# Performance work log

Hardware: AMD Instinct MI355X
Metric: run time of the kernel (lower is better)

The kernel has to match this reference:

```python
import jax, jax.numpy as jnp
import numpy as np
import math

B, T, D, V, M = 32, 2048, 512, 4096, 64
COVERAGE_FLOOR = 0.05
BIG = 1e30


def masked_median(values, mask):
    # values, mask: [B, T]; torch.median = lower median = sorted[(n-1)//2]
    valid = mask > 0.5
    n = valid.sum(axis=1)  # [B]
    s = jnp.sort(jnp.where(valid, values, BIG), axis=1)
    idx = jnp.maximum((n - 1) // 2, 0)
    med = jnp.take_along_axis(s, idx[:, None], axis=1)  # [B,1]
    return jnp.where(n[:, None] > 0, med, 0.0)


def masked_mean(values, mask):
    # values: [B,T,D], mask: [B,T]
    denom = jnp.maximum(mask.sum(axis=1, keepdims=True), 1.0)  # [B,1]
    return (values * mask[:, :, None]).sum(axis=1) / denom


def masked_std(values, mask, mean):
    denom = jnp.maximum(mask.sum(axis=1, keepdims=True), 1.0)
    diff2 = (values - mean[:, None, :]) ** 2 * mask[:, :, None]
    return jnp.sqrt(diff2.sum(axis=1) / jnp.maximum(denom, 1e-6) + 1e-6)


def conv1d(x, w, b):
    # x: [B,T,D], w: [K=3, I=D, O=D], padding=1 -> same length
    y = jax.lax.conv_general_dilated(x, w, window_strides=(1,), padding=[(1, 1)],
                                     dimension_numbers=('NHC', 'HIO', 'NHC'))
    return y + b


def layer_norm(x, w, b, eps=1e-5):
    mu = x.mean(axis=-1, keepdims=True)
    var = ((x - mu) ** 2).mean(axis=-1, keepdims=True)
    return (x - mu) * jax.lax.rsqrt(var + eps) * w + b


def setup_inputs() -> dict:
    key = jax.random.key(0)
    ks = jax.random.split(key, 20)
    units = jax.random.randint(ks[0], (B, T), 0, V)
    dur = jax.random.uniform(ks[1], (B, T), jnp.float32, 0.01, 2.0)
    valid = (jax.random.uniform(ks[2], (B, T)) > 0.1).astype(jnp.float32)
    speech = valid * (jax.random.uniform(ks[3], (B, T)) > 0.2).astype(jnp.float32)
    s = 0.02
    params = dict(
        emb=jax.random.normal(ks[4], (V, D)) * s,
        W_in=jax.random.normal(ks[5], (D + 2, D)) * s, b_in=jnp.zeros((D,)),
        W_c1=jax.random.normal(ks[6], (3, D, D)) * s, b_c1=jnp.zeros((D,)),
        W_c2=jax.random.normal(ks[7], (3, D, D)) * s, b_c2=jnp.zeros((D,)),
        ln_w=jnp.ones((D,)), ln_b=jnp.zeros((D,)),
        codebook_key=jax.random.normal(ks[8], (M, D)) * s,
        W_p1=jax.random.normal(ks[9], (2 * D, D)) * s, b_p1=jnp.zeros((D,)),
        W_p2=jax.random.normal(ks[10], (D, D)) * s, b_p2=jnp.zeros((D,)),
    )
    return dict(prompt_content_units=units, prompt_duration_obs=dur,
                prompt_valid_mask=valid, prompt_speech_mask=speech, **params)


def reference(prompt_content_units, prompt_duration_obs, prompt_valid_mask, prompt_speech_mask,
              emb, W_in, b_in, W_c1, b_c1, W_c2, b_c2, ln_w, ln_b,
              codebook_key, W_p1, b_p1, W_p2, b_p2):
    valid = jnp.clip(prompt_valid_mask, 0.0, 1.0)          # [B,T]
    speech = jnp.clip(prompt_speech_mask, 0.0, 1.0) * valid
    logdur = jnp.log(jnp.maximum(prompt_duration_obs, 1e-4)) * valid
    global_rate = masked_median(logdur, speech)             # [B,1]
    ref_residual = (logdur - global_rate) * valid            # [B,T]

    # encode prompt summary
    sil_flag = jnp.maximum(valid - speech, 0.0)
    h = jnp.concatenate([emb[prompt_content_units],
                         ref_residual[:, :, None], sil_flag[:, :, None]], axis=-1)
    h = h @ W_in + b_in                                      # [B,T,D]
    h = jax.nn.gelu(conv1d(h, W_c1, b_c1), approximate=False)
    h = jax.nn.gelu(conv1d(h, W_c2, b_c2), approximate=False)
    h = layer_norm(h, ln_w, ln_b) * valid[:, :, None]

    summary_mask = speech  # summary_pool_speech_only=True
    mean = masked_mean(h, summary_mask)                      # [B,D]
    std = masked_std(h, summary_mask, mean)                  # [B,D]
    z = jnp.concatenate([mean, std], axis=-1) @ W_p1 + b_p1
    summary_state = jnp.tanh(jax.nn.gelu(z, approximate=False) @ W_p2 + b_p2)
    support_raw = valid.sum(axis=1, keepdims=True)           # [B,1]
    support = jnp.maximum(support_raw, 1.0)
    summary_state = jnp.where(support_raw > 0.0, summary_state, 0.0)

    score = jnp.einsum('btd,md->btm', h, codebook_key) / math.sqrt(float(D))
    score = jnp.where(valid[:, :, None] <= 0.0, -10000.0, score)
    attn = jax.nn.softmax(score, axis=-1) * valid[:, :, None]  # [B,T,M]
    role_mass = attn.sum(axis=1)                               # [B,M]
    role_denom = jnp.maximum(role_mass, 1e-6)
    role_value = jnp.einsum('btm,bt->bm', attn, ref_residual) / role_denom
    diff2 = (ref_residual[:, :, None] - role_value[:, None, :]) ** 2  # [B,T,M]
    role_var = (attn * diff2).sum(axis=1) / role_denom
    role_var = jnp.maximum(jnp.where(role_mass > 0.0, role_var, 1e-4), 1e-4)
    role_coverage = jnp.maximum(role_mass / support, COVERAGE_FLOOR)
    prompt_role_fit = jnp.einsum('btm,bm->bt', attn, role_value) * valid

    return (global_rate, summary_state, role_value, role_var, role_coverage, prompt_role_fit)
```

## Files before the change

### kernel.cpp

```cpp
#include <hip/hip_runtime.h>
#include <hip/hip_bf16.h>
#include <math.h>


typedef unsigned short u16;
typedef unsigned char u8;
typedef __attribute__((ext_vector_type(8))) short short8;
typedef __attribute__((ext_vector_type(4))) float f32x4;
typedef __attribute__((ext_vector_type(4))) int int4v;
typedef __attribute__((ext_vector_type(8))) int int8v;

constexpr int B_ = 32, T_ = 2048, D_ = 512, V_ = 4096, M_ = 64, TP_ = 2050;

constexpr int OUT_GR = 0;
constexpr int OUT_SUM = 32;
constexpr int OUT_RV = 16416;
constexpr int OUT_VAR = 18464;
constexpr int OUT_COV = 20512;
constexpr int OUT_FIT = 22560;

constexpr size_t OFF_S0 = 0;
constexpr size_t OFF_S1 = OFF_S0 + 2048 * 4;
constexpr size_t OFF_S2 = OFF_S1 + 2048 * 4;
constexpr size_t OFF_SH = OFF_S2 + 2048 * 4;
constexpr size_t OFF_SH2 = OFF_SH + 16384 * 4;
constexpr size_t ZERO_BYTES = OFF_SH2 + 16384 * 4;
constexpr size_t OFF_RESID = ZERO_BYTES;
constexpr size_t OFF_GR = OFF_RESID + 65536 * 4;
constexpr size_t OFF_SUP = OFF_GR + 128;
constexpr size_t OFF_SPC = OFF_SUP + 128;
constexpr size_t OFF_RVW = OFF_SPC + 128;
constexpr size_t OFF_WTIN = OFF_RVW + 8192;
constexpr size_t OFF_WTC1 = OFF_WTIN + 524288;
constexpr size_t OFF_WTC2 = OFF_WTC1 + 786432;
constexpr size_t OFF_CKB = OFF_WTC2 + 786432;
constexpr size_t OFF_EMBB = OFF_CKB + 65536;
constexpr size_t OFF_TBL = OFF_EMBB + 4194304;
constexpr size_t OFF_H0 = OFF_TBL + 8388608;
constexpr size_t OFF_H1 = OFF_H0 + 33587200;
constexpr size_t OFF_H2 = OFF_H1 + 33587200;
constexpr size_t OFF_ATTN = OFF_H2 + 67108864;

__device__ __forceinline__ float clamp01(float x) { return fminf(fmaxf(x, 0.f), 1.f); }
__device__ __forceinline__ float b2f(u16 u) { return __uint_as_float(((unsigned)u) << 16); }
__device__ __forceinline__ u16 f2b(float f) {
  unsigned u = __float_as_uint(f);
  unsigned r = (u + 0x7FFFu + ((u >> 16) & 1u)) >> 16;
  return (u16)r;
}
__device__ __forceinline__ u8 f2fp8(float f) {
  return (u8)(__builtin_amdgcn_cvt_pk_fp8_f32(f, f, 0, false) & 0xFF);
}
__device__ __forceinline__ float gelu_f(float x) {
  return 0.5f * x * (1.0f + erff(x * 0.7071067811865475f));
}
__device__ __forceinline__ void gload16(const void* g, void* l) {
  __builtin_amdgcn_global_load_lds((const __attribute__((address_space(1))) void*)g,
                                   (__attribute__((address_space(3))) void*)l, 16, 0, 0);
}

__global__ __launch_bounds__(256) void median_kernel(
    const float* __restrict__ dur, const float* __restrict__ vmask,
    const float* __restrict__ smask, float* __restrict__ out0,
    float* __restrict__ gr, float* __restrict__ sup, float* __restrict__ spc,
    float* __restrict__ resid) {
  int b = blockIdx.x, tid = threadIdx.x;
  int wv = tid >> 6, lane = tid & 63;
  __shared__ float wredf[8];
  __shared__ int wredi[4];
  unsigned keys[8];
  float ldv[8], vmv[8];
  float vs = 0.f, ss = 0.f;
#pragma unroll
  for (int j = 0; j < 8; ++j) {
    int t = j * 256 + tid;
    float vm = clamp01(vmask[b * T_ + t]);
    float sm = clamp01(smask[b * T_ + t]) * vm;
    vs += vm; ss += sm;
    float ld = logf(fmaxf(dur[b * T_ + t], 1e-4f)) * vm;
    ldv[j] = ld; vmv[j] = vm;
    unsigned bits = __float_as_uint(ld);
    unsigned key = (bits & 0x80000000u) ? ~bits : (bits | 0x80000000u);
    keys[j] = (sm > 0.5f) ? key : 0xFFFFFFFFu;
  }
  for (int o = 32; o > 0; o >>= 1) { vs += __shfl_xor(vs, o); ss += __shfl_xor(ss, o); }
  if (lane == 0) { wredf[wv] = vs; wredf[4 + wv] = ss; }
  __syncthreads();
  float s_sup = wredf[0] + wredf[1] + wredf[2] + wredf[3];
  float s_spc = wredf[4] + wredf[5] + wredf[6] + wredf[7];
  int n = (int)(s_spc + 0.5f);
  int target = (n > 0) ? ((n - 1) / 2 + 1) : 1;
  unsigned lo = 0u, hi = 0xFFFFFFFFu;
  for (int it = 0; it < 32; ++it) {
    unsigned mid = lo + ((hi - lo) >> 1);
    int c = 0;
#pragma unroll
    for (int j = 0; j < 8; ++j) c += (keys[j] <= mid) ? 1 : 0;
    for (int o = 32; o > 0; o >>= 1) c += __shfl_xor(c, o);
    __syncthreads();
    if (lane == 0) wredi[wv] = c;
    __syncthreads();
    int tot = wredi[0] + wredi[1] + wredi[2] + wredi[3];
    if (tot >= target) hi = mid; else lo = mid + 1;
  }
  float med = 0.f;
  if (n > 0) {
    unsigned K = lo;
    unsigned ub = (K & 0x80000000u) ? (K & 0x7FFFFFFFu) : ~K;
    med = __uint_as_float(ub);
  }
  if (tid == 0) { out0[OUT_GR + b] = med; gr[b] = med; sup[b] = s_sup; spc[b] = s_spc; }
#pragma unroll
  for (int j = 0; j < 8; ++j) {
    int t = j * 256 + tid;
    resid[b * T_ + t] = (ldv[j] - med) * vmv[j];
  }
}

__global__ __launch_bounds__(256) void wpack_kernel(
    const float* __restrict__ W_in, const float* __restrict__ W_c1,
    const float* __restrict__ W_c2, u16* __restrict__ wtin,
    u8* __restrict__ wtc1, u8* __restrict__ wtc2) {
  __shared__ float tile[64][65];
  int x = blockIdx.x;
  int m = x >> 6, tl = x & 63;
  int kt = tl >> 3, nt = tl & 7;
  const float* src;
  if (m == 0) src = W_in;
  else if (m <= 3) src = W_c1 + (size_t)(m - 1) * 262144;
  else src = W_c2 + (size_t)(m - 4) * 262144;
  int tid = threadIdx.x;
#pragma unroll
  for (int j = 0; j < 16; ++j) {
    int idx = j * 256 + tid;
    int r = idx >> 6, c = idx & 63;
    tile[r][c] = src[(size_t)(kt * 64 + r) * 512 + nt * 64 + c];
  }
  __syncthreads();
  if (m == 0) {
#pragma unroll
    for (int j = 0; j < 16; ++j) {
      int idx = j * 256 + tid;
      int r = idx >> 6, c = idx & 63;
      wtin[(size_t)(nt * 64 + r) * 512 + kt * 64 + c] = f2b(tile[c][r]);
    }
  } else {
    u8* dst = (m <= 3) ? wtc1 + (size_t)(m - 1) * 262144
                       : wtc2 + (size_t)(m - 4) * 262144;
#pragma unroll
    for (int j = 0; j < 16; ++j) {
      int idx = j * 256 + tid;
      int r = idx >> 6, c = idx & 63;
      dst[(size_t)(nt * 64 + r) * 512 + kt * 64 + c] = f2fp8(tile[c][r] * 64.f);
    }
  }
}

__global__ __launch_bounds__(256) void convert_kernel(
    const float* __restrict__ ck, const float* __restrict__ emb,
    u16* __restrict__ ckb, u16* __restrict__ embb) {
  int idx = blockIdx.x * 256 + threadIdx.x;
  float4 v;
  u16* dst;
  if (idx < 8192) {
    v = reinterpret_cast<const float4*>(ck)[idx];
    dst = ckb + idx * 4;
  } else {
    int i = idx - 8192;
    v = reinterpret_cast<const float4*>(emb)[i];
    dst = embb + (size_t)i * 4;
  }
  uint2 o;
  o.x = (unsigned)f2b(v.x) | ((unsigned)f2b(v.y) << 16);
  o.y = (unsigned)f2b(v.z) | ((unsigned)f2b(v.w) << 16);
  *reinterpret_cast<uint2*>(dst) = o;
}

__global__ __launch_bounds__(256) void gemm_plain_kernel(
    const u16* __restrict__ A, const u16* __restrict__ Bt,
    const float* __restrict__ bias, u16* __restrict__ Cout) {
  __shared__ u16 ldsA[64 * 64];
  __shared__ u16 ldsB[128 * 64];
  const int tid = threadIdx.x;
  const int row0 = blockIdx.x * 64;
  const int col0 = blockIdx.y * 128;

  f32x4 acc[2][4] = {};
  const int wv = tid >> 6, lane = tid & 63;
  const int wr = (wv >> 1) << 5;
  const int wc = (wv & 1) << 6;
  const int lr = lane & 15, cgrp = lane >> 4;

  const u16* Ab = A + (size_t)row0 * 512;
  const u16* Bb = Bt + (size_t)col0 * 512;
  for (int k0 = 0; k0 < 512; k0 += 64) {
    if (k0) __syncthreads();
#pragma unroll
    for (int j = 0; j < 2; ++j) {
      int ci = j * 256 + tid;
      int r = ci >> 3, s = ci & 7;
      int gs = s ^ (r & 7);
      gload16(Ab + (size_t)r * 512 + k0 + gs * 8, &ldsA[ci * 8]);
    }
#pragma unroll
    for (int j = 0; j < 4; ++j) {
      int ci = j * 256 + tid;
      int r = ci >> 3, s = ci & 7;
      int gs = s ^ (r & 7);
      gload16(Bb + (size_t)r * 512 + k0 + gs * 8, &ldsB[ci * 8]);
    }
    __syncthreads();
#pragma unroll
    for (int kk = 0; kk < 2; ++kk) {
      short8 af[2], bfr[4];
#pragma unroll
      for (int m = 0; m < 2; ++m) {
        int r = wr + m * 16 + lr;
        int s = (kk * 4 + cgrp) ^ (r & 7);
        af[m] = *reinterpret_cast<const short8*>(&ldsA[(r << 6) + (s << 3)]);
      }
#pragma unroll
      for (int n = 0; n < 4; ++n) {
        int r = wc + n * 16 + lr;
        int s = (kk * 4 + cgrp) ^ (r & 7);
        bfr[n] = *reinterpret_cast<const short8*>(&ldsB[(r << 6) + (s << 3)]);
      }
#pragma unroll
      for (int m = 0; m < 2; ++m)
#pragma unroll
        for (int n = 0; n < 4; ++n)
          acc[m][n] = __builtin_amdgcn_mfma_f32_16x16x32_bf16(af[m], bfr[n], acc[m][n], 0, 0, 0);
    }
  }
#pragma unroll
  for (int m = 0; m < 2; ++m)
#pragma unroll
    for (int n = 0; n < 4; ++n)
#pragma unroll
      for (int r = 0; r < 4; ++r) {
        int lrow = wr + m * 16 + (lane >> 4) * 4 + r;
        int lcol = wc + n * 16 + (lane & 15);
        Cout[(size_t)(row0 + lrow) * 512 + col0 + lcol] =
            f2b(acc[m][n][r] + bias[col0 + lcol]);
      }
}

template <int PADOUT>
__global__ __launch_bounds__(256, 3) void conv_gemm_kernel(
    const u8* __restrict__ A, const u8* __restrict__ Bt,
    const float* __restrict__ bias, u8* __restrict__ Cout) {
  __shared__ u8 ldsA[130 * 128];
  __shared__ u8 ldsB[3 * 64 * 128];
  const int tid = threadIdx.x;
  const int id = blockIdx.x;
  const int wg = (id & 7) * 512 + (id >> 3);
  const int rb = wg >> 3, cb = wg & 7;
  const int row0 = rb * 128, col0 = cb * 64;
  const int b = row0 >> 11, t0 = row0 & 2047;
  const size_t aBase = ((size_t)b * TP_ + t0) * 512;
  const size_t oBase = PADOUT ? ((size_t)b * TP_ + 1 + t0) : (size_t)row0;

  f32x4 acc[4][2] = {};
  const int wv = tid >> 6, lane = tid & 63;
  const int wr = (wv >> 1) << 6;
  const int wc = (wv & 1) << 5;
  const int lr = lane & 15, cgrp = lane >> 4;

  const u8* Ab = A + aBase;
#pragma unroll 1
  for (int k0 = 0; k0 < 512; k0 += 128) {
    if (k0) __syncthreads();
#pragma unroll
    for (int j = 0; j < 5; ++j) {
      int ci = j * 256 + tid;
      if (ci < 1040) {
        int r = ci >> 3, s = ci & 7;
        int gs = s ^ (r & 7);
        gload16(Ab + (size_t)r * 512 + k0 + gs * 16, &ldsA[ci * 16]);
      }
    }
#pragma unroll
    for (int j = 0; j < 6; ++j) {
      int ci = j * 256 + tid;
      int r = ci >> 3, s = ci & 7;
      int tap = r >> 6, n = r & 63;
      int gs = s ^ (r & 7);
      gload16(Bt + ((size_t)(tap * 512 + col0 + n)) * 512 + k0 + gs * 16, &ldsB[ci * 16]);
    }
    __syncthreads();
#pragma unroll
    for (int tap = 0; tap < 3; ++tap) {
      int8v af[4], bfr[2];
#pragma unroll
      for (int m = 0; m < 4; ++m) {
        int r = wr + m * 16 + lr + tap;
        int s0 = (2 * cgrp) ^ (r & 7);
        int s1 = (2 * cgrp + 1) ^ (r & 7);
        int4v lo = *reinterpret_cast<const int4v*>(&ldsA[(r << 7) + (s0 << 4)]);
        int4v hi = *reinterpret_cast<const int4v*>(&ldsA[(r << 7) + (s1 << 4)]);
        af[m] = __builtin_shufflevector(lo, hi, 0, 1, 2, 3, 4, 5, 6, 7);
      }
#pragma unroll
      for (int n = 0; n < 2; ++n) {
        int rB = tap * 64 + wc + n * 16 + lr;
        int s0 = (2 * cgrp) ^ (rB & 7);
        int s1 = (2 * cgrp + 1) ^ (rB & 7);
        int4v lo = *reinterpret_cast<const int4v*>(&ldsB[(rB << 7) + (s0 << 4)]);
        int4v hi = *reinterpret_cast<const int4v*>(&ldsB[(rB << 7) + (s1 << 4)]);
        bfr[n] = __builtin_shufflevector(lo, hi, 0, 1, 2, 3, 4, 5, 6, 7);
      }
#pragma unroll
      for (int m = 0; m < 4; ++m)
#pragma unroll
        for (int n = 0; n < 2; ++n)
          acc[m][n] = __builtin_amdgcn_mfma_scale_f32_16x16x128_f8f6f4(
              af[m], bfr[n], acc[m][n], 0, 0, 0, 0x7F7F7F7F, 0, 0x7F7F7F7F);
    }
  }
#pragma unroll
  for (int m = 0; m < 4; ++m)
#pragma unroll
    for (int n = 0; n < 2; ++n)
#pragma unroll
      for (int r = 0; r < 4; ++r) {
        int lrow = wr + m * 16 + (lane >> 4) * 4 + r;
        int lcol = wc + n * 16 + (lane & 15);
        float v = acc[m][n][r] * (1.f / 4096.f) + bias[col0 + lcol];
        v = gelu_f(v);
        Cout[(oBase + lrow) * 512 + col0 + lcol] = f2fp8(v * 64.f);
      }
}

__global__ __launch_bounds__(256) void gather_kernel(
    const int* __restrict__ units, const float* __restrict__ resid,
    const float* __restrict__ vmask, const float* __restrict__ smask,
    const u16* __restrict__ tbl, const float* __restrict__ w512,
    const float* __restrict__ w513, u8* __restrict__ h0p, u8* __restrict__ h1p) {
  int row = blockIdx.x * 4 + (threadIdx.x >> 6);
  int b = row / TP_, tp = row - b * TP_;
  int lane = threadIdx.x & 63;
  size_t o = (size_t)row * 512 + lane * 8;
  if (tp == 0 || tp == TP_ - 1) {
    uint2 z = {0, 0};
    *reinterpret_cast<uint2*>(&h0p[o]) = z;
    *reinterpret_cast<uint2*>(&h1p[o]) = z;
    return;
  }
  int t = tp - 1, g = b * T_ + t;
  float vm = clamp01(vmask[g]);
  float sm = clamp01(smask[g]) * vm;
  float sil = fmaxf(vm - sm, 0.f);
  float rs = resid[g];
  int u = units[g];
  uint4 tv = *reinterpret_cast<const uint4*>(tbl + (size_t)u * 512 + lane * 8);
  float tr[8];
  tr[0] = __uint_as_float(tv.x << 16); tr[1] = __uint_as_float(tv.x & 0xFFFF0000u);
  tr[2] = __uint_as_float(tv.y << 16); tr[3] = __uint_as_float(tv.y & 0xFFFF0000u);
  tr[4] = __uint_as_float(tv.z << 16); tr[5] = __uint_as_float(tv.z & 0xFFFF0000u);
  tr[6] = __uint_as_float(tv.w << 16); tr[7] = __uint_as_float(tv.w & 0xFFFF0000u);
  const float* a = w512 + lane * 8;
  const float* c = w513 + lane * 8;
  float f[8];
#pragma unroll
  for (int j = 0; j < 8; ++j) f[j] = (tr[j] + rs * a[j] + sil * c[j]) * 64.f;
  unsigned lo = __builtin_amdgcn_cvt_pk_fp8_f32(f[0], f[1], 0, false);
  lo = __builtin_amdgcn_cvt_pk_fp8_f32(f[2], f[3], lo, true);
  unsigned hi = __builtin_amdgcn_cvt_pk_fp8_f32(f[4], f[5], 0, false);
  hi = __builtin_amdgcn_cvt_pk_fp8_f32(f[6], f[7], hi, true);
  uint2 val = {lo, hi};
  *reinterpret_cast<uint2*>(&h0p[o]) = val;
}

__global__ __launch_bounds__(256) void lnpool_kernel(
    const u8* __restrict__ hin, u16* __restrict__ hout,
    const float* __restrict__ lnw, const float* __restrict__ lnb,
    const float* __restrict__ vmask, const float* __restrict__ smask,
    float* __restrict__ Sh, float* __restrict__ Sh2) {
  int b = blockIdx.y, chunk = blockIdx.x, tid = threadIdx.x;
  int lane = tid & 63, tof = tid >> 6;
  __shared__ float shA[512], shQ[512];
  shA[tid] = 0.f; shA[tid + 256] = 0.f;
  shQ[tid] = 0.f; shQ[tid + 256] = 0.f;
  __syncthreads();
  int d8 = lane * 8;
  float wv_[8], bv_[8];
#pragma unroll
  for (int j = 0; j < 8; ++j) { wv_[j] = lnw[d8 + j]; bv_[j] = lnb[d8 + j]; }
  float a[8] = {}, q[8] = {};
  const float inv64 = 1.f / 64.f;
  for (int i = 0; i < 32; ++i) {
    int t = chunk * 128 + i * 4 + tof;
    int g = b * T_ + t;
    float vm = clamp01(vmask[g]);
    float sp = clamp01(smask[g]) * vm;
    const u8* p = hin + (size_t)g * 512 + d8;
    uint2 raw = *reinterpret_cast<const uint2*>(p);
    float x[8];
    x[0] = __builtin_amdgcn_cvt_f32_fp8(raw.x, 0) * inv64;
    x[1] = __builtin_amdgcn_cvt_f32_fp8(raw.x, 1) * inv64;
    x[2] = __builtin_amdgcn_cvt_f32_fp8(raw.x, 2) * inv64;
    x[3] = __builtin_amdgcn_cvt_f32_fp8(raw.x, 3) * inv64;
    x[4] = __builtin_amdgcn_cvt_f32_fp8(raw.y, 0) * inv64;
    x[5] = __builtin_amdgcn_cvt_f32_fp8(raw.y, 1) * inv64;
    x[6] = __builtin_amdgcn_cvt_f32_fp8(raw.y, 2) * inv64;
    x[7] = __builtin_amdgcn_cvt_f32_fp8(raw.y, 3) * inv64;
    float s = 0.f, sq = 0.f;
#pragma unroll
    for (int j = 0; j < 8; ++j) { s += x[j]; sq = fmaf(x[j], x[j], sq); }
    for (int o = 32; o > 0; o >>= 1) { s += __shfl_xor(s, o); sq += __shfl_xor(sq, o); }
    float mu = s * (1.f / 512.f);
    float var = fmaxf(sq * (1.f / 512.f) - mu * mu, 0.f);
    float rstd = rsqrtf(var + 1e-5f);
    u16 ob[8];
#pragma unroll
    for (int j = 0; j < 8; ++j) {
      float y = ((x[j] - mu) * rstd * wv_[j] + bv_[j]) * vm;
      ob[j] = f2b(y);
      a[j] = fmaf(y, sp, a[j]);
      q[j] = fmaf(y * y, sp, q[j]);
    }
    uint4 val;
    val.x = (unsigned)ob[0] | ((unsigned)ob[1] << 16);
    val.y = (unsigned)ob[2] | ((unsigned)ob[3] << 16);
    val.z = (unsigned)ob[4] | ((unsigned)ob[5] << 16);
    val.w = (unsigned)ob[6] | ((unsigned)ob[7] << 16);
    *reinterpret_cast<uint4*>(&hout[(size_t)g * 512 + d8]) = val;
  }
#pragma unroll
  for (int j = 0; j < 8; ++j) {
    atomicAdd(&shA[d8 + j], a[j]);
    atomicAdd(&shQ[d8 + j], q[j]);
  }
  __syncthreads();
  atomicAdd(&Sh[b * 512 + tid], shA[tid]);
  atomicAdd(&Sh[b * 512 + tid + 256], shA[tid + 256]);
  atomicAdd(&Sh2[b * 512 + tid], shQ[tid]);
  atomicAdd(&Sh2[b * 512 + tid + 256], shQ[tid + 256]);
}

__global__ __launch_bounds__(256) void score_kernel(
    const u16* __restrict__ h, const u16* __restrict__ ckb,
    const float* __restrict__ resid, const float* __restrict__ vmask,
    u16* __restrict__ attn, float* __restrict__ S0, float* __restrict__ S1,
    float* __restrict__ S2) {
  __shared__ char smem[98304];
  __shared__ float s0s[64], s1s[64], s2s[64];
  u16* ckl = (u16*)smem;
  u16* ldsH = (u16*)(smem + 65536);
  float* attn_lds = (float*)smem;

  const int tid = threadIdx.x;
  const int base = blockIdx.x * 256;
  const int bq = base >> 11;

#pragma unroll
  for (int it = 0; it < 16; ++it) {
    int ci = it * 256 + tid;
    int m = ci >> 6, s = ci & 63;
    int sw = (s & 56) | ((s & 7) ^ (m & 7));
    *reinterpret_cast<uint4*>(&ckl[(m << 9) + (sw << 3)]) =
        *reinterpret_cast<const uint4*>(&ckb[(m << 9) + (s << 3)]);
  }
  if (tid < 64) { s0s[tid] = 0.f; s1s[tid] = 0.f; s2s[tid] = 0.f; }

  const int wv = tid >> 6, lane = tid & 63;
  const int lr = lane & 15, cgrp = lane >> 4;
  const int hi = lane >> 4, lf = lane & 15;
  f32x4 acc[4][4] = {};

  const u16* hb = h + (size_t)base * 512;
  for (int k0 = 0; k0 < 512; k0 += 64) {
    __syncthreads();
#pragma unroll
    for (int j = 0; j < 8; ++j) {
      int ci = j * 256 + tid;
      int r = ci >> 3, s = ci & 7;
      int gs = s ^ (r & 7);
      gload16(hb + (size_t)r * 512 + k0 + gs * 8, &ldsH[ci * 8]);
    }
    __syncthreads();
#pragma unroll
    for (int kk = 0; kk < 2; ++kk) {
      short8 af[4], bfr[4];
#pragma unroll
      for (int m = 0; m < 4; ++m) {
        int r = wv * 64 + m * 16 + lr;
        int s = (kk * 4 + cgrp) ^ (r & 7);
        af[m] = *reinterpret_cast<const short8*>(&ldsH[(r << 6) + (s << 3)]);
      }
#pragma unroll
      for (int n = 0; n < 4; ++n) {
        int r = n * 16 + lr;
        int s = (kk * 4 + cgrp) ^ (r & 7);
        bfr[n] = *reinterpret_cast<const short8*>(&ckl[(r << 9) + k0 + (s << 3)]);
      }
#pragma unroll
      for (int m = 0; m < 4; ++m)
#pragma unroll
        for (int n = 0; n < 4; ++n)
          acc[m][n] = __builtin_amdgcn_mfma_f32_16x16x32_bf16(af[m], bfr[n], acc[m][n], 0, 0, 0);
    }
  }
  __syncthreads();

  const float scale = 0.04419417382415922f;
  float s0p[4] = {0.f, 0.f, 0.f, 0.f};
  float s1p[4] = {0.f, 0.f, 0.f, 0.f};
  float s2p[4] = {0.f, 0.f, 0.f, 0.f};
#pragma unroll
  for (int m = 0; m < 4; ++m) {
#pragma unroll
    for (int rr = 0; rr < 4; ++rr) {
      int tl = wv * 64 + m * 16 + hi * 4 + rr;
      int tg = base + tl;
      float v[4];
#pragma unroll
      for (int n = 0; n < 4; ++n) v[n] = acc[m][n][rr] * scale;
      float mx = fmaxf(fmaxf(v[0], v[1]), fmaxf(v[2], v[3]));
      mx = fmaxf(mx, __shfl_xor(mx, 1));
      mx = fmaxf(mx, __shfl_xor(mx, 2));
      mx = fmaxf(mx, __shfl_xor(mx, 4));
      mx = fmaxf(mx, __shfl_xor(mx, 8));
      float e[4], sum = 0.f;
#pragma unroll
      for (int n = 0; n < 4; ++n) { e[n] = expf(v[n] - mx); sum += e[n]; }
      sum += __shfl_xor(sum, 1);
      sum += __shfl_xor(sum, 2);
      sum += __shfl_xor(sum, 4);
      sum += __shfl_xor(sum, 8);
      float vm = clamp01(vmask[tg]);
      float inv = vm / sum;
      float rs = resid[tg];
#pragma unroll
      for (int n = 0; n < 4; ++n) {
        float aa = e[n] * inv;
        attn_lds[tl * 65 + n * 16 + lf] = aa;
        s0p[n] += aa; s1p[n] += aa * rs; s2p[n] += aa * rs * rs;
      }
    }
  }
#pragma unroll
  for (int n = 0; n < 4; ++n) {
    s0p[n] += __shfl_xor(s0p[n], 16); s0p[n] += __shfl_xor(s0p[n], 32);
    s1p[n] += __shfl_xor(s1p[n], 16); s1p[n] += __shfl_xor(s1p[n], 32);
    s2p[n] += __shfl_xor(s2p[n], 16); s2p[n] += __shfl_xor(s2p[n], 32);
  }
  if (hi == 0) {
#pragma unroll
    for (int n = 0; n < 4; ++n) {
      atomicAdd(&s0s[n * 16 + lf], s0p[n]);
      atomicAdd(&s1s[n * 16 + lf], s1p[n]);
      atomicAdd(&s2s[n * 16 + lf], s2p[n]);
    }
  }
  __syncthreads();
#pragma unroll
  for (int it = 0; it < 8; ++it) {
    int ci = it * 256 + tid;
    int tl = ci >> 3, c8 = (ci & 7) * 8;
    u16 ob[8];
#pragma unroll
    for (int j = 0; j < 8; ++j) ob[j] = f2b(attn_lds[tl * 65 + c8 + j]);
    uint4 val;
    val.x = (unsigned)ob[0] | ((unsigned)ob[1] << 16);
    val.y = (unsigned)ob[2] | ((unsigned)ob[3] << 16);
    val.z = (unsigned)ob[4] | ((unsigned)ob[5] << 16);
    val.w = (unsigned)ob[6] | ((unsigned)ob[7] << 16);
    *reinterpret_cast<uint4*>(&attn[(size_t)(base + tl) * 64 + c8]) = val;
  }
  if (tid < 64) {
    atomicAdd(&S0[bq * 64 + tid], s0s[tid]);
    atomicAdd(&S1[bq * 64 + tid], s1s[tid]);
    atomicAdd(&S2[bq * 64 + tid], s2s[tid]);
  }
}

__global__ __launch_bounds__(64) void role_kernel(
    const float* __restrict__ S0, const float* __restrict__ S1,
    const float* __restrict__ S2, const float* __restrict__ sup,
    float* __restrict__ out, float* __restrict__ rv) {
  int b = blockIdx.x, m = threadIdx.x;
  float mass = S0[b * 64 + m], s1 = S1[b * 64 + m], s2 = S2[b * 64 + m];
  float dn = fmaxf(mass, 1e-6f);
  float v = s1 / dn;
  float var = (s2 - 2.f * v * s1 + v * v * mass) / dn;
  var = fmaxf(var, 1e-4f);
  float support = fmaxf(sup[b], 1.f);
  float cov = fmaxf(mass / support, 0.05f);
  out[OUT_RV + b * 64 + m] = v;
  out[OUT_VAR + b * 64 + m] = var;
  out[OUT_COV + b * 64 + m] = cov;
  rv[b * 64 + m] = v;
}

__global__ __launch_bounds__(512) void mlp_kernel(
    const float* __restrict__ Sh, const float* __restrict__ Sh2,
    const float* __restrict__ spc, const float* __restrict__ sup,
    const float* __restrict__ Wp1, const float* __restrict__ bp1,
    const float* __restrict__ Wp2, const float* __restrict__ bp2,
    float* __restrict__ out) {
  int b = blockIdx.x, j = threadIdx.x;
  __shared__ float ms[1024];
  __shared__ float zg[512];
  float denom = fmaxf(spc[b], 1.0f);
  float mean = Sh[b * 512 + j] / denom;
  float ex2 = Sh2[b * 512 + j] / denom;
  float var = fmaxf(ex2 - mean * mean, 0.f);
  ms[j] = mean;
  ms[512 + j] = sqrtf(var + 1e-6f);
  __syncthreads();
  float z0 = 0.f, z1 = 0.f, z2 = 0.f, z3 = 0.f;
  for (int k = 0; k < 1024; k += 4) {
    z0 = fmaf(ms[k], Wp1[(size_t)k * 512 + j], z0);
    z1 = fmaf(ms[k + 1], Wp1[(size_t)(k + 1) * 512 + j], z1);
    z2 = fmaf(ms[k + 2], Wp1[(size_t)(k + 2) * 512 + j], z2);
    z3 = fmaf(ms[k + 3], Wp1[(size_t)(k + 3) * 512 + j], z3);
  }
  float z = bp1[j] + ((z0 + z1) + (z2 + z3));
  zg[j] = gelu_f(z);
  __syncthreads();
  float o0 = 0.f, o1 = 0.f, o2 = 0.f, o3 = 0.f;
  for (int k = 0; k < 512; k += 4) {
    o0 = fmaf(zg[k], Wp2[(size_t)k * 512 + j], o0);
    o1 = fmaf(zg[k + 1], Wp2[(size_t)(k + 1) * 512 + j], o1);
    o2 = fmaf(zg[k + 2], Wp2[(size_t)(k + 2) * 512 + j], o2);
    o3 = fmaf(zg[k + 3], Wp2[(size_t)(k + 3) * 512 + j], o3);
  }
  float o = bp2[j] + ((o0 + o1) + (o2 + o3));
  float sm = tanhf(o);
  out[OUT_SUM + b * 512 + j] = (sup[b] > 0.f) ? sm : 0.f;
}

__global__ __launch_bounds__(256) void fit_kernel(
    const u16* __restrict__ attn, const float* __restrict__ rv,
    const float* __restrict__ vmask, float* __restrict__ out) {
  int tid = threadIdx.x;
  int wv = tid >> 6, lane = tid & 63;
  int t = blockIdx.x * 4 + wv;
  int b = t >> 11;
  float a = b2f(attn[(size_t)t * 64 + lane]) * rv[b * 64 + lane];
  for (int o = 32; o > 0; o >>= 1) a += __shfl_xor(a, o);
  if (lane == 0) out[OUT_FIT + t] = a * clamp01(vmask[t]);
}

extern "C" void kernel_launch(void* const* d_in, const int* in_sizes, int n_in,
                              void* d_out, int out_size, void* d_ws, size_t ws_size,
                              hipStream_t stream) {
  (void)in_sizes; (void)n_in; (void)out_size; (void)ws_size;
  const int* units = (const int*)d_in[0];
  const float* dur = (const float*)d_in[1];
  const float* vmask = (const float*)d_in[2];
  const float* smask = (const float*)d_in[3];
  const float* emb = (const float*)d_in[4];
  const float* W_in = (const float*)d_in[5];
  const float* b_in = (const float*)d_in[6];
  const float* W_c1 = (const float*)d_in[7];
  const float* b_c1 = (const float*)d_in[8];
  const float* W_c2 = (const float*)d_in[9];
  const float* b_c2 = (const float*)d_in[10];
  const float* ln_w = (const float*)d_in[11];
  const float* ln_b = (const float*)d_in[12];
  const float* ck = (const float*)d_in[13];
  const float* W_p1 = (const float*)d_in[14];
  const float* b_p1 = (const float*)d_in[15];
  const float* W_p2 = (const float*)d_in[16];
  const float* b_p2 = (const float*)d_in[17];
  float* out = (float*)d_out;

  char* w = (char*)d_ws;
  float* S0 = (float*)(w + OFF_S0);
  float* S1 = (float*)(w + OFF_S1);
  float* S2 = (float*)(w + OFF_S2);
  float* Sh = (float*)(w + OFF_SH);
  float* Sh2 = (float*)(w + OFF_SH2);
  float* resid = (float*)(w + OFF_RESID);
  float* gr = (float*)(w + OFF_GR);
  float* sup = (float*)(w + OFF_SUP);
  float* spc = (float*)(w + OFF_SPC);
  float* rv = (float*)(w + OFF_RVW);
  u16* wtin = (u16*)(w + OFF_WTIN);
  u8* wtc1 = (u8*)(w + OFF_WTC1);
  u8* wtc2 = (u8*)(w + OFF_WTC2);
  u16* ckb = (u16*)(w + OFF_CKB);
  u16* embb = (u16*)(w + OFF_EMBB);
  u16* tbl = (u16*)(w + OFF_TBL);
  u8* h0p = (u8*)(w + OFF_H0);
  u8* h1p = (u8*)(w + OFF_H1);
  u8* h2f = (u8*)(w + OFF_H2);
  u16* h2b = (u16*)(w + OFF_H0);
  u16* attn = (u16*)(w + OFF_ATTN);

  hipMemsetAsync(d_ws, 0, ZERO_BYTES, stream);
  median_kernel<<<B_, 256, 0, stream>>>(dur, vmask, smask, out, gr, sup, spc, resid);
  wpack_kernel<<<448, 256, 0, stream>>>(W_in, W_c1, W_c2, wtin, wtc1, wtc2);
  convert_kernel<<<2080, 256, 0, stream>>>(ck, emb, ckb, embb);
  gemm_plain_kernel<<<dim3(64, 4), 256, 0, stream>>>(embb, wtin, b_in, tbl);
  gather_kernel<<<B_ * TP_ / 4, 256, 0, stream>>>(units, resid, vmask, smask, tbl,
                                                  W_in + 512 * 512, W_in + 513 * 512, h0p, h1p);
  conv_gemm_kernel<1><<<4096, 256, 0, stream>>>(h0p, wtc1, b_c1, h1p);
  conv_gemm_kernel<0><<<4096, 256, 0, stream>>>(h1p, wtc2, b_c2, h2f);
  lnpool_kernel<<<dim3(16, 32), 256, 0, stream>>>(h2f, h2b, ln_w, ln_b, vmask, smask, Sh, Sh2);
  score_kernel<<<256, 256, 0, stream>>>(h2b, ckb, resid, vmask, attn, S0, S1, S2);
  role_kernel<<<B_, 64, 0, stream>>>(S0, S1, S2, sup, out, rv);
  mlp_kernel<<<B_, 512, 0, stream>>>(Sh, Sh2, spc, sup, W_p1, b_p1, W_p2, b_p2, out);
  fit_kernel<<<B_ * T_ / 4, 256, 0, stream>>>(attn, rv, vmask, out);
}
```

Measured before the change: 304.0 us.

## Precompute conv GEMM offsets and shrink score kernel tiles and LDS

In the conv GEMM kernel, the global-load and LDS-fragment offsets are now computed once before the K loop and kept in registers, which removes repeated index arithmetic but raises register pressure. The score kernel now handles 128 rows per block instead of 256 and launches twice as many blocks. It no longer stages the codebook in LDS and reads B fragments straight from global memory (cached), and it stores the attention tile as bf16 in LDS. This cuts LDS use from about 96KB so more blocks can be resident and the 256-CU device is better filled, at the cost of uncoalesced global reads for the codebook.

```diff
diff --git a/kernel.cpp b/kernel.cpp
--- a/kernel.cpp
+++ b/kernel.cpp
@@ -266,6 +266,41 @@
   const int wc = (wv & 1) << 5;
   const int lr = lane & 15, cgrp = lane >> 4;
 
+  unsigned goffA[5];
+#pragma unroll
+  for (int j = 0; j < 5; ++j) {
+    int ci = j * 256 + tid;
+    int cc = (ci < 1040) ? ci : 1039;
+    int r = cc >> 3, s = cc & 7;
+    int gs = s ^ (r & 7);
+    goffA[j] = (unsigned)(r * 512 + gs * 16);
+  }
+  unsigned goffB[6];
+#pragma unroll
+  for (int j = 0; j < 6; ++j) {
+    int ci = j * 256 + tid;
+    int r = ci >> 3, s = ci & 7;
+    int tap = r >> 6, n = r & 63;
+    int gs = s ^ (r & 7);
+    goffB[j] = (unsigned)((tap * 512 + col0 + n) * 512 + gs * 16);
+  }
+  unsigned aoff0[3][4], aoff1[3][4], boff0[3][2], boff1[3][2];
+#pragma unroll
+  for (int tap = 0; tap < 3; ++tap) {
+#pragma unroll
+    for (int m = 0; m < 4; ++m) {
+      int r = wr + m * 16 + lr + tap;
+      aoff0[tap][m] = (unsigned)((r << 7) + ((((2 * cgrp)) ^ (r & 7)) << 4));
+      aoff1[tap][m] = (unsigned)((r << 7) + ((((2 * cgrp + 1)) ^ (r & 7)) << 4));
+    }
+#pragma unroll
+    for (int n = 0; n < 2; ++n) {
+      int rB = tap * 64 + wc + n * 16 + lr;
+      boff0[tap][n] = (unsigned)((rB << 7) + ((((2 * cgrp)) ^ (rB & 7)) << 4));
+      boff1[tap][n] = (unsigned)((rB << 7) + ((((2 * cgrp + 1)) ^ (rB & 7)) << 4));
+    }
+  }
+
   const u8* Ab = A + aBase;
 #pragma unroll 1
   for (int k0 = 0; k0 < 512; k0 += 128) {
@@ -273,40 +308,25 @@
 #pragma unroll
     for (int j = 0; j < 5; ++j) {
       int ci = j * 256 + tid;
-      if (ci < 1040) {
-        int r = ci >> 3, s = ci & 7;
-        int gs = s ^ (r & 7);
-        gload16(Ab + (size_t)r * 512 + k0 + gs * 16, &ldsA[ci * 16]);
-      }
-    }
-#pragma unroll
-    for (int j = 0; j < 6; ++j) {
-      int ci = j * 256 + tid;
-      int r = ci >> 3, s = ci & 7;
-      int tap = r >> 6, n = r & 63;
-      int gs = s ^ (r & 7);
-      gload16(Bt + ((size_t)(tap * 512 + col0 + n)) * 512 + k0 + gs * 16, &ldsB[ci * 16]);
-    }
+      if (ci < 1040) gload16(Ab + goffA[j] + k0, &ldsA[ci * 16]);
+    }
+#pragma unroll
+    for (int j = 0; j < 6; ++j)
+      gload16(Bt + goffB[j] + k0, &ldsB[(j * 256 + tid) * 16]);
     __syncthreads();
 #pragma unroll
     for (int tap = 0; tap < 3; ++tap) {
       int8v af[4], bfr[2];
 #pragma unroll
       for (int m = 0; m < 4; ++m) {
-        int r = wr + m * 16 + lr + tap;
-        int s0 = (2 * cgrp) ^ (r & 7);
-        int s1 = (2 * cgrp + 1) ^ (r & 7);
-        int4v lo = *reinterpret_cast<const int4v*>(&ldsA[(r << 7) + (s0 << 4)]);
-        int4v hi = *reinterpret_cast<const int4v*>(&ldsA[(r << 7) + (s1 << 4)]);
+        int4v lo = *reinterpret_cast<const int4v*>(&ldsA[aoff0[tap][m]]);
+        int4v hi = *reinterpret_cast<const int4v*>(&ldsA[aoff1[tap][m]]);
         af[m] = __builtin_shufflevector(lo, hi, 0, 1, 2, 3, 4, 5, 6, 7);
       }
 #pragma unroll
       for (int n = 0; n < 2; ++n) {
-        int rB = tap * 64 + wc + n * 16 + lr;
-        int s0 = (2 * cgrp) ^ (rB & 7);
-        int s1 = (2 * cgrp + 1) ^ (rB & 7);
-        int4v lo = *reinterpret_cast<const int4v*>(&ldsB[(rB << 7) + (s0 << 4)]);
-        int4v hi = *reinterpret_cast<const int4v*>(&ldsB[(rB << 7) + (s1 << 4)]);
+        int4v lo = *reinterpret_cast<const int4v*>(&ldsB[boff0[tap][n]]);
+        int4v hi = *reinterpret_cast<const int4v*>(&ldsB[boff1[tap][n]]);
         bfr[n] = __builtin_shufflevector(lo, hi, 0, 1, 2, 3, 4, 5, 6, 7);
       }
 #pragma unroll
@@ -443,36 +463,26 @@
     const float* __restrict__ resid, const float* __restrict__ vmask,
     u16* __restrict__ attn, float* __restrict__ S0, float* __restrict__ S1,
     float* __restrict__ S2) {
-  __shared__ char smem[98304];
+  __shared__ u16 ldsH[128 * 64];
+  __shared__ u16 attn_lds[128 * 65];
   __shared__ float s0s[64], s1s[64], s2s[64];
-  u16* ckl = (u16*)smem;
-  u16* ldsH = (u16*)(smem + 65536);
-  float* attn_lds = (float*)smem;
 
   const int tid = threadIdx.x;
-  const int base = blockIdx.x * 256;
+  const int base = blockIdx.x * 128;
   const int bq = base >> 11;
 
-#pragma unroll
-  for (int it = 0; it < 16; ++it) {
-    int ci = it * 256 + tid;
-    int m = ci >> 6, s = ci & 63;
-    int sw = (s & 56) | ((s & 7) ^ (m & 7));
-    *reinterpret_cast<uint4*>(&ckl[(m << 9) + (sw << 3)]) =
-        *reinterpret_cast<const uint4*>(&ckb[(m << 9) + (s << 3)]);
-  }
   if (tid < 64) { s0s[tid] = 0.f; s1s[tid] = 0.f; s2s[tid] = 0.f; }
 
   const int wv = tid >> 6, lane = tid & 63;
   const int lr = lane & 15, cgrp = lane >> 4;
   const int hi = lane >> 4, lf = lane & 15;
-  f32x4 acc[4][4] = {};
+  f32x4 acc[2][4] = {};
 
   const u16* hb = h + (size_t)base * 512;
   for (int k0 = 0; k0 < 512; k0 += 64) {
     __syncthreads();
 #pragma unroll
-    for (int j = 0; j < 8; ++j) {
+    for (int j = 0; j < 4; ++j) {
       int ci = j * 256 + tid;
       int r = ci >> 3, s = ci & 7;
       int gs = s ^ (r & 7);
@@ -481,21 +491,21 @@
     __syncthreads();
 #pragma unroll
     for (int kk = 0; kk < 2; ++kk) {
-      short8 af[4], bfr[4];
-#pragma unroll
-      for (int m = 0; m < 4; ++m) {
-        int r = wv * 64 + m * 16 + lr;
+      short8 af[2], bfr[4];
+#pragma unroll
+      for (int m = 0; m < 2; ++m) {
+        int r = wv * 32 + m * 16 + lr;
         int s = (kk * 4 + cgrp) ^ (r & 7);
         af[m] = *reinterpret_cast<const short8*>(&ldsH[(r << 6) + (s << 3)]);
       }
 #pragma unroll
       for (int n = 0; n < 4; ++n) {
-        int r = n * 16 + lr;
-        int s = (kk * 4 + cgrp) ^ (r & 7);
-        bfr[n] = *reinterpret_cast<const short8*>(&ckl[(r << 9) + k0 + (s << 3)]);
-      }
-#pragma unroll
-      for (int m = 0; m < 4; ++m)
+        int rB = n * 16 + lr;
+        bfr[n] = *reinterpret_cast<const short8*>(
+            &ckb[(size_t)rB * 512 + k0 + (kk * 4 + cgrp) * 8]);
+      }
+#pragma unroll
+      for (int m = 0; m < 2; ++m)
 #pragma unroll
         for (int n = 0; n < 4; ++n)
           acc[m][n] = __builtin_amdgcn_mfma_f32_16x16x32_bf16(af[m], bfr[n], acc[m][n], 0, 0, 0);
@@ -508,10 +518,10 @@
   float s1p[4] = {0.f, 0.f, 0.f, 0.f};
   float s2p[4] = {0.f, 0.f, 0.f, 0.f};
 #pragma unroll
-  for (int m = 0; m < 4; ++m) {
+  for (int m = 0; m < 2; ++m) {
 #pragma unroll
     for (int rr = 0; rr < 4; ++rr) {
-      int tl = wv * 64 + m * 16 + hi * 4 + rr;
+      int tl = wv * 32 + m * 16 + hi * 4 + rr;
       int tg = base + tl;
       float v[4];
 #pragma unroll
@@ -534,7 +544,7 @@
 #pragma unroll
       for (int n = 0; n < 4; ++n) {
         float aa = e[n] * inv;
-        attn_lds[tl * 65 + n * 16 + lf] = aa;
+        attn_lds[tl * 65 + n * 16 + lf] = f2b(aa);
         s0p[n] += aa; s1p[n] += aa * rs; s2p[n] += aa * rs * rs;
       }
     }
@@ -555,12 +565,12 @@
   }
   __syncthreads();
 #pragma unroll
-  for (int it = 0; it < 8; ++it) {
+  for (int it = 0; it < 4; ++it) {
     int ci = it * 256 + tid;
     int tl = ci >> 3, c8 = (ci & 7) * 8;
     u16 ob[8];
 #pragma unroll
-    for (int j = 0; j < 8; ++j) ob[j] = f2b(attn_lds[tl * 65 + c8 + j]);
+    for (int j = 0; j < 8; ++j) ob[j] = attn_lds[tl * 65 + c8 + j];
     uint4 val;
     val.x = (unsigned)ob[0] | ((unsigned)ob[1] << 16);
     val.y = (unsigned)ob[2] | ((unsigned)ob[3] << 16);
@@ -700,7 +710,7 @@
   conv_gemm_kernel<1><<<4096, 256, 0, stream>>>(h0p, wtc1, b_c1, h1p);
   conv_gemm_kernel<0><<<4096, 256, 0, stream>>>(h1p, wtc2, b_c2, h2f);
   lnpool_kernel<<<dim3(16, 32), 256, 0, stream>>>(h2f, h2b, ln_w, ln_b, vmask, smask, Sh, Sh2);
-  score_kernel<<<256, 256, 0, stream>>>(h2b, ckb, resid, vmask, attn, S0, S1, S2);
+  score_kernel<<<512, 256, 0, stream>>>(h2b, ckb, resid, vmask, attn, S0, S1, S2);
   role_kernel<<<B_, 64, 0, stream>>>(S0, S1, S2, sup, out, rv);
   mlp_kernel<<<B_, 512, 0, stream>>>(Sh, Sh2, spc, sup, W_p1, b_p1, W_p2, b_p2, out);
   fit_kernel<<<B_ * T_ / 4, 256, 0, stream>>>(attn, rv, vmask, out);
```

New measurement: 306.2 us. No clear change (+0.7%).
